# Optimization experiments

Measured on AMD Instinct MI355X. Metric: run time of the kernel, lower is better.

## Reference

```python
import jax, jax.numpy as jnp
import numpy as np

EPS = 0.1           # sinkhorn entropic regularizer (epsilon=0.1 in OT())
GAMMA = 1.0         # KL penalty on relaxed (row) marginal (gamma=1)
NUM_SK_ITERS = 3    # num_iters=3, final=False path
RHO_UPPER = 1.0
RHO_BASE = 0.1


def sigmoid_rampup(current, rampup_length):
    if rampup_length == 0:
        return 1.0
    current = np.clip(current, 0.0, rampup_length)
    phase = 1.0 - current / rampup_length
    return float(np.exp(-5.0 * phase * phase))


def set_rho(current, total):
    rho = sigmoid_rampup(current, total) * RHO_UPPER + RHO_BASE
    return min(rho, 1.0)


def setup_inputs() -> dict:
    key = jax.random.key(0)
    kx, ky = jax.random.split(key)
    x = jax.random.normal(kx, (8192, 1024), dtype=jnp.float32)
    y = jax.random.normal(ky, (2048, 1024), dtype=jnp.float32)
    return {"x": x, "y": y, "iterations": 100, "iterations_per_epoch": 20}


def _normalize_feature(x):
    # x = x - x.min(-1)[0].unsqueeze(-1)
    return x - jnp.min(x, axis=-1, keepdims=True)


def _cdist(x, y):
    # torch.cdist with p=2 (Euclidean)
    x2 = jnp.sum(x * x, axis=-1, keepdims=True)          # (N,1)
    y2 = jnp.sum(y * y, axis=-1)                         # (M,)
    d2 = x2 + y2[None, :] - 2.0 * (x @ y.T)              # (N,M)
    return jnp.sqrt(jnp.maximum(d2, 0.0))


def _semi_sinkhorn_stable(cost, rho):
    """Log-domain (stable) semi-relaxed Sinkhorn-Knopp.
    Column marginal is enforced exactly with total mass rho (curriculum mass);
    row marginal is relaxed via KL penalty gamma -> damped f update.
    Returns transport plan with sum(flow) == rho."""
    N, M = cost.shape
    lam = GAMMA / (GAMMA + EPS)
    loga = -np.log(N)                   # uniform row prior (prior=None)
    logb = np.log(rho) - np.log(M)      # uniform column marginal, mass rho
    logK = -cost / EPS                  # (N,M)
    f = jnp.zeros((N,), cost.dtype)
    g = jnp.zeros((M,), cost.dtype)
    lse = jax.scipy.special.logsumexp
    for _ in range(NUM_SK_ITERS):
        f = -lam * EPS * lse(logK + g[None, :] / EPS + logb, axis=1)
        g = -EPS * lse(logK + f[:, None] / EPS + loga, axis=0)
    flow = jnp.exp(logK + f[:, None] / EPS + g[None, :] / EPS + loga + logb)
    return flow


def reference(x, y, iterations, iterations_per_epoch):
    x = _normalize_feature(x)
    y = _normalize_feature(y)
    rho = set_rho(iterations, 10 * iterations_per_epoch)  # sigmoid rho schedule
    cost = _cdist(x, y)
    cost = cost / jnp.max(cost)
    flow = _semi_sinkhorn_stable(cost, rho)
    flow = flow / rho                                      # renormalize to total mass 1
    dist = jnp.sum(cost * flow)
    return flow, dist
```

## Files before the change

### kernel.cpp

```cpp
#include <hip/hip_runtime.h>
#include <math.h>

#define N_ROWS 8192
#define M_COLS 2048
#define K_DIM  1024
#define NM     ((size_t)N_ROWS * M_COLS)

#define LAM       0.9090909090909091f
#define LOG_M     7.624618986159398f

#define SKB 1024
#define RPB (N_ROWS / SKB)

typedef __bf16 bf16x8 __attribute__((ext_vector_type(8)));
typedef float  f32x4  __attribute__((ext_vector_type(4)));
typedef unsigned short u16x8 __attribute__((ext_vector_type(8)));
typedef _Float16 h8 __attribute__((ext_vector_type(8)));


static __device__ __forceinline__ size_t xb_off(int i) {
    return ((size_t)(i >> 1) << 13) + 4096 + ((size_t)(i & 1) << 11);
}
static __device__ __forceinline__ size_t yb_off(int j) {
    return ((size_t)1 << 25) + ((size_t)(j >> 1) << 13) + 4096 + ((size_t)(j & 1) << 11);
}

static __device__ __forceinline__ unsigned pk_bf16(float a, float b) {
#if __has_builtin(__builtin_amdgcn_cvt_pk_bf16_f32)
    typedef __bf16 bf16x2 __attribute__((ext_vector_type(2)));
    bf16x2 r = __builtin_amdgcn_cvt_pk_bf16_f32(a, b);
    return __builtin_bit_cast(unsigned, r);
#else
    unsigned ua = __float_as_uint(a), ub = __float_as_uint(b);
    ua += 0x7FFFu + ((ua >> 16) & 1u);
    ub += 0x7FFFu + ((ub >> 16) & 1u);
    return (ua >> 16) | (ub & 0xFFFF0000u);
#endif
}

static __device__ __forceinline__ bf16x8 lds_frag(const unsigned short* p) {
    return __builtin_bit_cast(bf16x8, *(const u16x8*)p);
}

static __device__ __forceinline__ void gload16(const void* g, void* l) {
    __builtin_amdgcn_global_load_lds(
        (const __attribute__((address_space(1))) unsigned int*)g,
        (__attribute__((address_space(3))) unsigned int*)l, 16, 0, 0);
}

__global__ __launch_bounds__(256) void rowstats_cvt(
    const float* __restrict__ X, const float* __restrict__ Y,
    unsigned char* __restrict__ outb,
    const int* __restrict__ iters, const int* __restrict__ ipe,
    float* __restrict__ params, float* __restrict__ sigma,
    unsigned int* __restrict__ d2max, float* __restrict__ dist,
    float* __restrict__ mx, float* __restrict__ sx, float* __restrict__ x2,
    float* __restrict__ my, float* __restrict__ sy, float* __restrict__ y2)
{
    const int b = blockIdx.x, tid = threadIdx.x;

    if (b == 0) {
        #pragma unroll 1
        for (int i = tid; i < 3 * M_COLS; i += 256) sigma[i] = 0.0f;
        if (tid == 0) {
            float ramp = 10.0f * (float)ipe[0];
            float rho;
            if (ramp == 0.0f) {
                rho = 1.1f;
            } else {
                float cur = fminf(fmaxf((float)iters[0], 0.0f), ramp);
                float phase = 1.0f - cur / ramp;
                rho = expf(-5.0f * phase * phase) + 0.1f;
            }
            rho = fminf(rho, 1.0f);
            params[0] = rho;
            params[1] = logf(rho) - LOG_M;
            *d2max = 0u;
            *dist = 0.0f;
        }
    }

    const bool isX = b < N_ROWS;
    const int row = isX ? b : b - N_ROWS;
    const float* src = isX ? (X + (size_t)row * K_DIM) : (Y + (size_t)row * K_DIM);
    const float4 v = ((const float4*)src)[tid];

    uint2 p; p.x = pk_bf16(v.x, v.y); p.y = pk_bf16(v.z, v.w);
    size_t off = isX ? xb_off(row) : yb_off(row);
    *(uint2*)(outb + off + (size_t)tid * 8) = p;

    float lmin = fminf(fminf(v.x, v.y), fminf(v.z, v.w));
    float lsum = v.x + v.y + v.z + v.w;
    float lsq  = v.x*v.x + v.y*v.y + v.z*v.z + v.w*v.w;

    __shared__ float rmin[256], rsum[256], rsq[256];
    rmin[tid] = lmin; rsum[tid] = lsum; rsq[tid] = lsq;
    __syncthreads();
    for (int s = 128; s > 0; s >>= 1) {
        if (tid < s) {
            rmin[tid] = fminf(rmin[tid], rmin[tid + s]);
            rsum[tid] += rsum[tid + s];
            rsq[tid]  += rsq[tid + s];
        }
        __syncthreads();
    }
    if (tid == 0) {
        float m = rmin[0], s = rsum[0], q = rsq[0];
        if (isX) { mx[row] = m; sx[row] = s; x2[row] = q - 2.f*m*s + (float)K_DIM*m*m; }
        else     { my[row] = m; sy[row] = s; y2[row] = q - 2.f*m*s + (float)K_DIM*m*m; }
    }
}

__global__ __launch_bounds__(512, 2) void gemm_cost_mfma(
    float* __restrict__ gbuf,
    const float* __restrict__ mx, const float* __restrict__ sx, const float* __restrict__ x2,
    const float* __restrict__ my, const float* __restrict__ sy, const float* __restrict__ y2,
    unsigned int* __restrict__ d2max)
{
    __shared__ unsigned short Ash[2][256 * 64];
    __shared__ unsigned short Bsh[2][256 * 64];
    __shared__ float rmax[512];

    const unsigned char* outb = (const unsigned char*)gbuf;
    const int tid  = threadIdx.x;
    const int lane = tid & 63;
    const int wave = tid >> 6;
    const int wm   = wave >> 2;
    const int wn   = wave & 3;
    const int r16  = lane & 15;
    const int q    = lane >> 4;

    const int bid0 = blockIdx.x;
    const int bid  = (bid0 & 7) * 32 + (bid0 >> 3);
    const int i0 = (bid >> 3) * 256, j0 = (bid & 7) * 256;

    const int srow  = tid >> 3;
    const int sslot = tid & 7;
    const int chS   = (sslot ^ (srow & 7)) * 16;

    f32x4 acc[8][4];
    #pragma unroll
    for (int u = 0; u < 8; ++u)
        #pragma unroll
        for (int v = 0; v < 4; ++v) acc[u][v] = (f32x4){0.f, 0.f, 0.f, 0.f};

    bf16x8 af[8], bfr[4];

#define STAGE(t2, s) do {                                                      \
        const int kb = (t2) * 128;                                             \
        _Pragma("unroll")                                                      \
        for (int g = 0; g < 4; ++g) {                                          \
            const int rw = g * 64 + srow;                                      \
            gload16(outb + xb_off(i0 + rw) + kb + chS,                         \
                    &Ash[s][g * 4096 + wave * 512]);                           \
            gload16(outb + yb_off(j0 + rw) + kb + chS,                         \
                    &Bsh[s][g * 4096 + wave * 512]);                           \
        }                                                                      \
    } while (0)

#define FRAGS(s, kk) do {                                                      \
        _Pragma("unroll")                                                      \
        for (int mi = 0; mi < 8; ++mi) {                                       \
            const int rA = wm * 128 + mi * 16 + r16;                           \
            af[mi] = lds_frag(&Ash[s][rA * 64 + (((kk)*4 + q) ^ (rA & 7)) * 8]); \
        }                                                                      \
        _Pragma("unroll")                                                      \
        for (int ni = 0; ni < 4; ++ni) {                                       \
            const int rB = wn * 64 + ni * 16 + r16;                            \
            bfr[ni] = lds_frag(&Bsh[s][rB * 64 + (((kk)*4 + q) ^ (rB & 7)) * 8]); \
        }                                                                      \
    } while (0)

#define MMAS() do {                                                            \
        _Pragma("unroll")                                                      \
        for (int mi = 0; mi < 8; ++mi)                                         \
            _Pragma("unroll")                                                  \
            for (int ni = 0; ni < 4; ++ni)                                     \
                acc[mi][ni] = __builtin_amdgcn_mfma_f32_16x16x32_bf16(         \
                    af[mi], bfr[ni], acc[mi][ni], 0, 0, 0);                    \
    } while (0)

    STAGE(0, 0);
    STAGE(1, 1);

    #pragma unroll 1
    for (int t = 0; t < 16; ++t) {
        const int side = t & 1;
        if (t < 15) asm volatile("s_waitcnt vmcnt(8)" ::: "memory");
        else        asm volatile("s_waitcnt vmcnt(0)" ::: "memory");
        __builtin_amdgcn_s_barrier();
        __builtin_amdgcn_sched_barrier(0);

        FRAGS(side, 0);
        asm volatile("s_waitcnt lgkmcnt(0)" ::: "memory");
        __builtin_amdgcn_sched_barrier(0);
        __builtin_amdgcn_s_setprio(1); MMAS(); __builtin_amdgcn_s_setprio(0);

        FRAGS(side, 1);
        asm volatile("s_waitcnt lgkmcnt(0)" ::: "memory");
        __builtin_amdgcn_sched_barrier(0);
        __builtin_amdgcn_s_barrier();
        __builtin_amdgcn_sched_barrier(0);
        if (t <= 13) STAGE(t + 2, side);
        __builtin_amdgcn_s_setprio(1); MMAS(); __builtin_amdgcn_s_setprio(0);
    }

#undef STAGE
#undef FRAGS
#undef MMAS

    _Float16* costh = (_Float16*)gbuf;
    float lmax = 0.0f;
    float myj[4], syj[4], yy[4];
    int jb[4];
    #pragma unroll
    for (int ni = 0; ni < 4; ++ni) {
        jb[ni] = j0 + wn * 64 + ni * 16 + r16;
        myj[ni] = my[jb[ni]]; syj[ni] = sy[jb[ni]]; yy[ni] = y2[jb[ni]];
    }
    #pragma unroll
    for (int mi = 0; mi < 8; ++mi) {
        #pragma unroll
        for (int reg = 0; reg < 4; ++reg) {
            const int i = i0 + wm * 128 + mi * 16 + q * 4 + reg;
            const float mxi = mx[i], sxi = sx[i], xxi = x2[i];
            #pragma unroll
            for (int ni = 0; ni < 4; ++ni) {
                float corr = mxi * syj[ni] + myj[ni] * sxi - (float)K_DIM * mxi * myj[ni];
                float d2 = xxi + yy[ni] - 2.0f * acc[mi][ni][reg] + 2.0f * corr;
                d2 = fmaxf(d2, 0.0f);
                lmax = fmaxf(lmax, d2);
                costh[(size_t)i * 4096 + jb[ni]] = (_Float16)sqrtf(d2);
            }
        }
    }
    rmax[tid] = lmax;
    __syncthreads();
    for (int s = 256; s > 0; s >>= 1) {
        if (tid < s) rmax[tid] = fmaxf(rmax[tid], rmax[tid + s]);
        __syncthreads();
    }
    if (tid == 0) atomicMax(d2max, __float_as_uint(rmax[0]));
}

template<int IT>
__global__ __launch_bounds__(256, 4) void sk_pass(
    const float* __restrict__ outbuf, const float* __restrict__ sigma,
    _Float16* __restrict__ gpart, float* __restrict__ w,
    const float* __restrict__ params, const unsigned int* __restrict__ d2max)
{
    __shared__ _Float16 Esh[RPB * M_COLS];
    __shared__ float R[RPB][4];
    __shared__ float W[RPB];

    const int tid  = threadIdx.x;
    const int lane = tid & 63;
    const int wave = tid >> 6;
    const int r0   = blockIdx.x * RPB;
    const float logb = params[1];
    const float invC10 = 10.0f * rsqrtf(__uint_as_float(*d2max));

    float u8[8];
    if constexpr (IT == 0) {
        #pragma unroll
        for (int c = 0; c < 8; ++c) u8[c] = 1.0f;
    } else {
        const float* sg = sigma + (IT - 1) * M_COLS;
        const float4 sa = *(const float4*)(sg + 8 * tid);
        const float4 sb = *(const float4*)(sg + 8 * tid + 4);
        u8[0] = (float)N_ROWS / sa.x; u8[1] = (float)N_ROWS / sa.y;
        u8[2] = (float)N_ROWS / sa.z; u8[3] = (float)N_ROWS / sa.w;
        u8[4] = (float)N_ROWS / sb.x; u8[5] = (float)N_ROWS / sb.y;
        u8[6] = (float)N_ROWS / sb.z; u8[7] = (float)N_ROWS / sb.w;
    }

    const _Float16* Cb = (const _Float16*)outbuf;
    float pr[RPB];
    #pragma unroll
    for (int r = 0; r < RPB; ++r) {
        h8 c = __builtin_bit_cast(h8, *(const uint4*)(Cb + (size_t)(r0 + r) * 4096 + 8 * tid));
        h8 e;
        float s = 0.0f;
        #pragma unroll
        for (int k = 0; k < 8; ++k) {
            _Float16 ek = (_Float16)__expf(-(float)c[k] * invC10);
            e[k] = ek;
            s += (float)ek * u8[k];
        }
        *(uint4*)&Esh[r * M_COLS + 8 * tid] = __builtin_bit_cast(uint4, e);
        pr[r] = s;
    }

    #pragma unroll
    for (int r = 0; r < RPB; ++r)
        #pragma unroll
        for (int off = 32; off > 0; off >>= 1)
            pr[r] += __shfl_xor(pr[r], off, 64);

    if (lane == 0)
        #pragma unroll
        for (int r = 0; r < RPB; ++r) R[r][wave] = pr[r];
    __syncthreads();
    if (tid < RPB) {
        float t = R[tid][0] + R[tid][1] + R[tid][2] + R[tid][3];
        float wr = __expf(-LAM * (logb + __logf(t)));
        W[tid] = wr;
        if constexpr (IT == 2) w[r0 + tid] = wr;
    }
    __syncthreads();

    float p[8] = {0.f, 0.f, 0.f, 0.f, 0.f, 0.f, 0.f, 0.f};
    #pragma unroll
    for (int r = 0; r < RPB; ++r) {
        h8 e = __builtin_bit_cast(h8, *(const uint4*)&Esh[r * M_COLS + 8 * tid]);
        const float wr = W[r];
        #pragma unroll
        for (int k = 0; k < 8; ++k) p[k] += (float)e[k] * wr;
    }
    h8 ph;
    #pragma unroll
    for (int k = 0; k < 8; ++k) ph[k] = (_Float16)p[k];
    *(uint4*)(gpart + (size_t)blockIdx.x * M_COLS + 8 * tid) = __builtin_bit_cast(uint4, ph);
}

__global__ __launch_bounds__(256) void sk_gred(
    const _Float16* __restrict__ gpart, float* __restrict__ sigma)
{
    const int col = (blockIdx.x & 7) * 256 + threadIdx.x;
    const int b0  = (blockIdx.x >> 3) * (SKB / 16);
    float s = 0.0f;
    #pragma unroll 8
    for (int b = 0; b < SKB / 16; ++b)
        s += (float)gpart[(size_t)(b0 + b) * M_COLS + col];
    atomicAdd(&sigma[col], s);
}

__global__ __launch_bounds__(256, 4) void flow_dist(
    float* __restrict__ outbuf, const float* __restrict__ w,
    const float* __restrict__ sigma2, const unsigned int* __restrict__ d2max,
    float* __restrict__ dist)
{
    __shared__ _Float16 Csh[RPB * M_COLS];
    __shared__ float W[RPB];
    __shared__ float red[256];

    const int tid = threadIdx.x;
    const int r0  = blockIdx.x * RPB;
    const float invNM = 1.0f / ((float)N_ROWS * (float)M_COLS);
    const float invC10 = 10.0f * rsqrtf(__uint_as_float(*d2max));
    const float inv01  = 0.1f * invC10;
    const _Float16* Cb = (const _Float16*)outbuf;

    #pragma unroll
    for (int r = 0; r < RPB; ++r) {
        uint4 cv = *(const uint4*)(Cb + (size_t)(r0 + r) * 4096 + 8 * tid);
        *(uint4*)&Csh[r * M_COLS + 8 * tid] = cv;
    }

    if (tid < RPB) W[tid] = w[r0 + tid];

    const float4 sA = *(const float4*)(sigma2 + 8 * tid);
    const float4 sB = *(const float4*)(sigma2 + 8 * tid + 4);
    float u8[8];
    u8[0] = (float)N_ROWS / sA.x; u8[1] = (float)N_ROWS / sA.y;
    u8[2] = (float)N_ROWS / sA.z; u8[3] = (float)N_ROWS / sA.w;
    u8[4] = (float)N_ROWS / sB.x; u8[5] = (float)N_ROWS / sB.y;
    u8[6] = (float)N_ROWS / sB.z; u8[7] = (float)N_ROWS / sB.w;

    __syncthreads();

    float local = 0.0f;
    #pragma unroll
    for (int r = 0; r < RPB; ++r) {
        h8 c = __builtin_bit_cast(h8, *(const uint4*)&Csh[r * M_COLS + 8 * tid]);
        const float wr = W[r];
        float fl[8];
        #pragma unroll
        for (int k = 0; k < 8; ++k) {
            float cst = (float)c[k];
            float e = __expf(-cst * invC10);
            float o = e * wr * u8[k] * invNM;
            fl[k] = o;
            local += (cst * inv01) * o;
        }
        float4 o0 = {fl[0], fl[1], fl[2], fl[3]};
        float4 o1 = {fl[4], fl[5], fl[6], fl[7]};
        float* frow = outbuf + (size_t)(r0 + r) * M_COLS + 8 * tid;
        *(float4*)frow = o0;
        *(float4*)(frow + 4) = o1;
    }

    red[tid] = local;
    __syncthreads();
    for (int s = 128; s > 0; s >>= 1) {
        if (tid < s) red[tid] += red[tid + s];
        __syncthreads();
    }
    if (tid == 0) atomicAdd(dist, red[0]);
}

extern "C" void kernel_launch(void* const* d_in, const int* in_sizes, int n_in,
                              void* d_out, int out_size, void* d_ws, size_t ws_size,
                              hipStream_t stream)
{
    const float* x     = (const float*)d_in[0];
    const float* y     = (const float*)d_in[1];
    const int*   iters = (const int*)d_in[2];
    const int*   ipe   = (const int*)d_in[3];
    float* out = (float*)d_out;
    float* ws  = (float*)d_ws;

    float*        params = ws;
    unsigned int* d2max  = (unsigned int*)(ws + 8);
    float* w     = ws + 16;
    float* sigma = w + N_ROWS;
    float* mx = sigma + 3 * M_COLS;
    float* sx = mx + N_ROWS;
    float* x2 = sx + N_ROWS;
    float* my = x2 + N_ROWS;
    float* sy = my + M_COLS;
    float* y2 = sy + M_COLS;
    _Float16* gpart = (_Float16*)(y2 + M_COLS);

    float* sigma0 = sigma;
    float* sigma1 = sigma + M_COLS;
    float* sigma2 = sigma + 2 * M_COLS;

    float* dist = out + NM;

    rowstats_cvt<<<N_ROWS + M_COLS, 256, 0, stream>>>(
        x, y, (unsigned char*)out, iters, ipe, params, sigma, d2max, dist,
        mx, sx, x2, my, sy, y2);
    gemm_cost_mfma<<<(N_ROWS / 256) * (M_COLS / 256), 512, 0, stream>>>(
        out, mx, sx, x2, my, sy, y2, d2max);

    sk_pass<0><<<SKB, 256, 0, stream>>>(out, sigma, gpart, w, params, d2max);
    sk_gred<<<128, 256, 0, stream>>>(gpart, sigma0);
    sk_pass<1><<<SKB, 256, 0, stream>>>(out, sigma, gpart, w, params, d2max);
    sk_gred<<<128, 256, 0, stream>>>(gpart, sigma1);
    sk_pass<2><<<SKB, 256, 0, stream>>>(out, sigma, gpart, w, params, d2max);
    sk_gred<<<128, 256, 0, stream>>>(gpart, sigma2);

    flow_dist<<<SKB, 256, 0, stream>>>(out, w, sigma2, d2max, dist);
}
```

Baseline: 207.6 us.

## Split GEMM main loop into four barrier-synchronized phases with staggered global prefetch

Restructures the bf16 MFMA main loop into four phases per K-tile, each loading half the A fragments (and the B fragments every other phase) before running 16 MFMAs. Global-to-LDS staging is split so half of the next tile's A rows are issued early and the rest are interleaved into the last phase, with vmcnt adjusted to match. The aim is to cut fragment register pressure and overlap LDS reads and global loads more finely with MFMA work. In exchange it adds more barriers per iteration, and the more intricate buffer reuse ordering raises the risk of LDS hazards.

New measurement: 210.8 us. Within noise of the previous version (+1.5%).

```diff
diff --git a/kernel.cpp b/kernel.cpp
--- a/kernel.cpp
+++ b/kernel.cpp
@@ -144,70 +144,70 @@
         #pragma unroll
         for (int v = 0; v < 4; ++v) acc[u][v] = (f32x4){0.f, 0.f, 0.f, 0.f};
 
-    bf16x8 af[8], bfr[4];
-
-#define STAGE(t2, s) do {                                                      \
-        const int kb = (t2) * 128;                                             \
+#define STG_A(s, g, t2) gload16(outb + xb_off(i0 + (g) * 64 + srow) + (t2) * 128 + chS, \
+                                &Ash[s][(g) * 4096 + wave * 512])
+#define STG_B(s, g, t2) gload16(outb + yb_off(j0 + (g) * 64 + srow) + (t2) * 128 + chS, \
+                                &Bsh[s][(g) * 4096 + wave * 512])
+
+#define PHASE(s, kk, mh, READB, STAGECODE) do {                                \
         _Pragma("unroll")                                                      \
-        for (int g = 0; g < 4; ++g) {                                          \
-            const int rw = g * 64 + srow;                                      \
-            gload16(outb + xb_off(i0 + rw) + kb + chS,                         \
-                    &Ash[s][g * 4096 + wave * 512]);                           \
-            gload16(outb + yb_off(j0 + rw) + kb + chS,                         \
-                    &Bsh[s][g * 4096 + wave * 512]);                           \
+        for (int i = 0; i < 4; ++i) {                                          \
+            const int rA = wm * 128 + ((mh) * 4 + i) * 16 + r16;               \
+            a_[i] = lds_frag(&Ash[s][rA * 64 + (((kk) * 4 + q) ^ (rA & 7)) * 8]); \
         }                                                                      \
-    } while (0)
-
-#define FRAGS(s, kk) do {                                                      \
+        if (READB) {                                                           \
+            _Pragma("unroll")                                                  \
+            for (int ni = 0; ni < 4; ++ni) {                                   \
+                const int rB = wn * 64 + ni * 16 + r16;                        \
+                b_[ni] = lds_frag(&Bsh[s][rB * 64 + (((kk) * 4 + q) ^ (rB & 7)) * 8]); \
+            }                                                                  \
+        }                                                                      \
+        STAGECODE;                                                             \
+        __builtin_amdgcn_s_barrier();                                          \
+        asm volatile("s_waitcnt lgkmcnt(0)" ::: "memory");                     \
+        __builtin_amdgcn_sched_barrier(0);                                     \
+        __builtin_amdgcn_s_setprio(1);                                         \
         _Pragma("unroll")                                                      \
-        for (int mi = 0; mi < 8; ++mi) {                                       \
-            const int rA = wm * 128 + mi * 16 + r16;                           \
-            af[mi] = lds_frag(&Ash[s][rA * 64 + (((kk)*4 + q) ^ (rA & 7)) * 8]); \
-        }                                                                      \
-        _Pragma("unroll")                                                      \
-        for (int ni = 0; ni < 4; ++ni) {                                       \
-            const int rB = wn * 64 + ni * 16 + r16;                            \
-            bfr[ni] = lds_frag(&Bsh[s][rB * 64 + (((kk)*4 + q) ^ (rB & 7)) * 8]); \
-        }                                                                      \
-    } while (0)
-
-#define MMAS() do {                                                            \
-        _Pragma("unroll")                                                      \
-        for (int mi = 0; mi < 8; ++mi)                                         \
+        for (int i = 0; i < 4; ++i)                                            \
             _Pragma("unroll")                                                  \
             for (int ni = 0; ni < 4; ++ni)                                     \
-                acc[mi][ni] = __builtin_amdgcn_mfma_f32_16x16x32_bf16(         \
-                    af[mi], bfr[ni], acc[mi][ni], 0, 0, 0);                    \
+                acc[(mh) * 4 + i][ni] = __builtin_amdgcn_mfma_f32_16x16x32_bf16( \
+                    a_[i], b_[ni], acc[(mh) * 4 + i][ni], 0, 0, 0);            \
+        __builtin_amdgcn_s_setprio(0);                                         \
+        __builtin_amdgcn_s_barrier();                                          \
     } while (0)
 
-    STAGE(0, 0);
-    STAGE(1, 1);
+    STG_A(0, 0, 0); STG_A(0, 1, 0); STG_A(0, 2, 0); STG_A(0, 3, 0);
+    STG_B(0, 0, 0); STG_B(0, 1, 0); STG_B(0, 2, 0); STG_B(0, 3, 0);
+    STG_A(1, 0, 1); STG_A(1, 2, 1);
+    STG_B(1, 0, 1); STG_B(1, 1, 1); STG_B(1, 2, 1); STG_B(1, 3, 1);
 
     #pragma unroll 1
     for (int t = 0; t < 16; ++t) {
         const int side = t & 1;
-        if (t < 15) asm volatile("s_waitcnt vmcnt(8)" ::: "memory");
+        if (t < 15) asm volatile("s_waitcnt vmcnt(6)" ::: "memory");
         else        asm volatile("s_waitcnt vmcnt(0)" ::: "memory");
         __builtin_amdgcn_s_barrier();
         __builtin_amdgcn_sched_barrier(0);
 
-        FRAGS(side, 0);
-        asm volatile("s_waitcnt lgkmcnt(0)" ::: "memory");
-        __builtin_amdgcn_sched_barrier(0);
-        __builtin_amdgcn_s_setprio(1); MMAS(); __builtin_amdgcn_s_setprio(0);
-
-        FRAGS(side, 1);
-        asm volatile("s_waitcnt lgkmcnt(0)" ::: "memory");
-        __builtin_amdgcn_sched_barrier(0);
-        __builtin_amdgcn_s_barrier();
-        __builtin_amdgcn_sched_barrier(0);
-        if (t <= 13) STAGE(t + 2, side);
-        __builtin_amdgcn_s_setprio(1); MMAS(); __builtin_amdgcn_s_setprio(0);
-    }
-
-#undef STAGE
-#undef FRAGS
-#undef MMAS
+        bf16x8 a_[4], b_[4];
+        PHASE(side, 0, 0, 1, {
+            if (t <= 14) { STG_A(side ^ 1, 1, t + 1); STG_A(side ^ 1, 3, t + 1); }
+        });
+        PHASE(side, 0, 1, 0, {});
+        PHASE(side, 1, 0, 1, {});
+        PHASE(side, 1, 1, 0, {
+            if (t <= 13) {
+                STG_A(side, 0, t + 2); STG_A(side, 2, t + 2);
+                STG_B(side, 0, t + 2); STG_B(side, 1, t + 2);
+                STG_B(side, 2, t + 2); STG_B(side, 3, t + 2);
+            }
+        });
+    }
+
+#undef PHASE
+#undef STG_A
+#undef STG_B
 
     _Float16* costh = (_Float16*)gbuf;
     float lmax = 0.0f;
```
